# Performance work log

Hardware: AMD Instinct MI355X
Metric: run time of the kernel (lower is better)

## Reference

```python
import jax, jax.numpy as jnp
import numpy as np

B, S, I, O = 8, 2048, 64, 64

def setup_inputs() -> dict:
    key = jax.random.key(0)
    k1, k2 = jax.random.split(key)
    x = jax.random.uniform(k1, (B, S, I), dtype=jnp.float32)
    kernel = jax.random.uniform(k2, (I, O), dtype=jnp.float32)
    return {"x": x, "kernel": kernel}

def reference(x, kernel):
    # Original: for i in I, for j in O: max(x[:,:,i], kernel[i,j]), concat j then i
    # => broadcasted max, i-major / j-minor flattening.
    b, s, i = x.shape
    o = kernel.shape[1]
    out = jnp.maximum(x[:, :, :, None], kernel[None, None, :, :])  # (B,S,I,O)
    return out.reshape(b, s, i * o)
```

## Files before the change

### kernel.cpp

```cpp
#include <hip/hip_runtime.h>


__global__ __launch_bounds__(256, 4) void fuzzy_max_kernel(
    const float* __restrict__ x,
    const float* __restrict__ km,
    float4* __restrict__ out,
    unsigned total4) {
  __shared__ float4 kf[1024];

  const unsigned t = threadIdx.x;
  const float4* km4 = reinterpret_cast<const float4*>(km);
#pragma unroll
  for (int it = 0; it < 4; ++it) {
    kf[t + 256u * it] = km4[t + 256u * it];
  }
  __syncthreads();

  const unsigned stride = gridDim.x * blockDim.x;
  for (unsigned v = blockIdx.x * blockDim.x + t; v < total4; v += stride) {
    const unsigned row = v >> 10;
    const unsigned rem = v & 1023u;
    const unsigned i = rem >> 4;
    const float xv = x[(row << 6) | i];
    const float4 k = kf[rem];
    float4 o;
    o.x = fmaxf(xv, k.x);
    o.y = fmaxf(xv, k.y);
    o.z = fmaxf(xv, k.z);
    o.w = fmaxf(xv, k.w);
    out[v] = o;
  }
}

extern "C" void kernel_launch(void* const* d_in, const int* in_sizes, int n_in,
                              void* d_out, int out_size, void* d_ws, size_t ws_size,
                              hipStream_t stream) {
  const float* x = reinterpret_cast<const float*>(d_in[0]);
  const float* km = reinterpret_cast<const float*>(d_in[1]);
  float4* out = reinterpret_cast<float4*>(d_out);

  const unsigned total4 = (unsigned)(out_size / 4);
  const int block = 256;
  const int grid = 4096;
  fuzzy_max_kernel<<<grid, block, 0, stream>>>(x, km, out, total4);
}
```

Measured before the change: 267.6 us.

## Hoist kernel values into registers, use nontemporal stores, double grid

Drops the shared-memory staging of the kernel matrix. Each thread now loads its fixed float4 of kernel values once into registers, which works because the grid stride is a multiple of 1024, so the column index never changes inside the loop. Output writes become nontemporal stores so the 256 MB streaming output bypasses cache retention. The grid doubles to 8192 blocks and the occupancy hint is removed. The register-hoisted path depends on the stride being divisible by 1024.

```diff
diff --git a/kernel.cpp b/kernel.cpp
--- a/kernel.cpp
+++ b/kernel.cpp
@@ -1,34 +1,32 @@
 #include <hip/hip_runtime.h>
 
 
-__global__ __launch_bounds__(256, 4) void fuzzy_max_kernel(
+typedef float v4f __attribute__((ext_vector_type(4)));
+
+__global__ __launch_bounds__(256) void fuzzy_max_kernel(
     const float* __restrict__ x,
     const float* __restrict__ km,
-    float4* __restrict__ out,
+    float* __restrict__ out,
     unsigned total4) {
-  __shared__ float4 kf[1024];
+  const unsigned v0 = blockIdx.x * blockDim.x + threadIdx.x;
+  const unsigned rem = v0 & 1023u;
+  const unsigned i = rem >> 4;
 
-  const unsigned t = threadIdx.x;
-  const float4* km4 = reinterpret_cast<const float4*>(km);
-#pragma unroll
-  for (int it = 0; it < 4; ++it) {
-    kf[t + 256u * it] = km4[t + 256u * it];
-  }
-  __syncthreads();
+  const v4f k = reinterpret_cast<const v4f*>(km)[rem];
 
   const unsigned stride = gridDim.x * blockDim.x;
-  for (unsigned v = blockIdx.x * blockDim.x + t; v < total4; v += stride) {
-    const unsigned row = v >> 10;
-    const unsigned rem = v & 1023u;
-    const unsigned i = rem >> 4;
+  const unsigned rowstep = stride >> 10;
+  unsigned row = v0 >> 10;
+
+  v4f* out4 = reinterpret_cast<v4f*>(out);
+  for (unsigned v = v0; v < total4; v += stride, row += rowstep) {
     const float xv = x[(row << 6) | i];
-    const float4 k = kf[rem];
-    float4 o;
+    v4f o;
     o.x = fmaxf(xv, k.x);
     o.y = fmaxf(xv, k.y);
     o.z = fmaxf(xv, k.z);
     o.w = fmaxf(xv, k.w);
-    out[v] = o;
+    __builtin_nontemporal_store(o, &out4[v]);
   }
 }
 
@@ -37,10 +35,10 @@
                               hipStream_t stream) {
   const float* x = reinterpret_cast<const float*>(d_in[0]);
   const float* km = reinterpret_cast<const float*>(d_in[1]);
-  float4* out = reinterpret_cast<float4*>(d_out);
+  float* out = reinterpret_cast<float*>(d_out);
 
   const unsigned total4 = (unsigned)(out_size / 4);
   const int block = 256;
-  const int grid = 4096;
+  const int grid = 8192;
   fuzzy_max_kernel<<<grid, block, 0, stream>>>(x, km, out, total4);
 }
```

New measurement: 272.8 us. No clear change (+2.0%).
